# Optimization experiments

Measured on AMD Instinct MI355X. Metric: run time of the kernel, lower is better.

The kernel has to match this reference:

```python
import jax, jax.numpy as jnp
import numpy as np
from jax import lax

K = 3  # deform kernel size (forced by shape consistency of the offset branch)


def conv2d(x, w, b, pad):
    y = lax.conv_general_dilated(x, w, (1, 1), [(pad, pad), (pad, pad)],
                                 dimension_numbers=('NCHW', 'OIHW', 'NCHW'))
    return y + b[None, :, None, None]


def deform_conv(x, offset, w):
    # Deformable conv v1, stride 1, pad 0, per-group offsets, zero outside borders.
    B, Cin, H, W = x.shape
    Cout = w.shape[0]
    Ho, Wo = H - K + 1, W - K + 1
    G = offset.shape[1] // (2 * K * K)  # num deformable groups (= cin // c_p_g)
    cpg = Cin // G
    # offset layout: [B, G, K*K, 2(y,x), Ho, Wo]
    off = offset.reshape(B, G, K * K, 2, Ho, Wo)
    ky = (jnp.arange(K * K) // K).astype(x.dtype)
    kx = (jnp.arange(K * K) % K).astype(x.dtype)
    py = off[:, :, :, 0] + jnp.arange(Ho, dtype=x.dtype)[None, None, None, :, None] + ky[None, None, :, None, None]
    px = off[:, :, :, 1] + jnp.arange(Wo, dtype=x.dtype)[None, None, None, None, :] + kx[None, None, :, None, None]
    y0 = jnp.floor(py)
    x0 = jnp.floor(px)
    fy = (py - y0)[..., None]  # [B,G,KK,Ho,Wo,1]
    fx = (px - x0)[..., None]
    y0i = y0.astype(jnp.int32)
    x0i = x0.astype(jnp.int32)
    xr = x.reshape(B, G, cpg, H, W)
    bi = jnp.arange(B)[:, None, None, None, None]
    gi = jnp.arange(G)[None, :, None, None, None]

    def gather(iy, ix):
        valid = (iy >= 0) & (iy < H) & (ix >= 0) & (ix < W)
        v = xr[bi, gi, :, jnp.clip(iy, 0, H - 1), jnp.clip(ix, 0, W - 1)]  # [B,G,KK,Ho,Wo,cpg]
        return v * valid[..., None].astype(x.dtype)

    v = ((1 - fy) * (1 - fx) * gather(y0i, x0i)
         + (1 - fy) * fx * gather(y0i, x0i + 1)
         + fy * (1 - fx) * gather(y0i + 1, x0i)
         + fy * fx * gather(y0i + 1, x0i + 1))
    # [B,G,KK,Ho,Wo,cpg] -> [B, Cin*K*K, Ho, Wo] matching weight layout [Cout, Cin, K, K]
    cols = v.transpose(0, 1, 5, 2, 3, 4).reshape(B, Cin * K * K, Ho, Wo)
    return jnp.einsum('ok,bkhw->bohw', w.reshape(Cout, -1), cols)


def setup_inputs() -> dict:
    key = jax.random.key(0)
    ks = jax.random.split(key, 8)
    B, cin, cout, H, W = 4, 64, 64, 130, 130
    s = 0.05
    x = jax.random.normal(ks[0], (B, cin, H, W), jnp.float32)
    w0 = jax.random.normal(ks[1], (cin, cin, 3, 3), jnp.float32) * s
    b0 = jnp.zeros((cin,), jnp.float32)
    w1 = jax.random.normal(ks[2], (cin // 2, cin, 1, 1), jnp.float32) * s
    b1 = jnp.zeros((cin // 2,), jnp.float32)
    w2 = jax.random.normal(ks[3], (cin // 2, cin // 2, 3, 3), jnp.float32) * s
    b2 = jnp.zeros((cin // 2,), jnp.float32)
    off_ch = cin * 2 * K * K  # c_p_g = 1 -> G = cin
    w3 = jax.random.normal(ks[4], (off_ch, cin // 2, 1, 1), jnp.float32) * s
    b3 = jnp.zeros((off_ch,), jnp.float32)
    wd = jax.random.normal(ks[5], (cout, cin, K, K), jnp.float32) * s
    return {"x": x, "w0": w0, "b0": b0, "w1": w1, "b1": b1, "w2": w2, "b2": b2,
            "w3": w3, "b3": b3, "wd": wd}


def reference(x, w0, b0, w1, b1, w2, b2, w3, b3, wd):
    t = conv2d(x, w0, b0, 0)                                   # [B,cin,H-2,W-2]
    t = lax.reduce_window(t, -jnp.inf, lax.max, (1, 1, 2, 2), (1, 1, 2, 2), 'VALID')
    t = conv2d(t, w1, b1, 0)
    t = conv2d(t, w2, b2, 1)
    t = conv2d(t, w3, b3, 0)                                   # offset logits
    t = jnp.repeat(jnp.repeat(t, 2, axis=2), 2, axis=3)        # nearest x2 upsample
    return deform_conv(x, t, wd)
```

## Files before the change

### kernel.cpp

```cpp
#include <hip/hip_runtime.h>
#include <hip/hip_bf16.h>
#include <hip/hip_fp16.h>


#define HX 130
#define WX 130

typedef short bf16x8 __attribute__((ext_vector_type(8)));
typedef _Float16 f16x8 __attribute__((ext_vector_type(8)));
typedef float f32x4 __attribute__((ext_vector_type(4)));

static __device__ __forceinline__ unsigned short f2bf(float f) {
    unsigned u = __float_as_uint(f);
    unsigned r = u + 0x7fff + ((u >> 16) & 1);
    return (unsigned short)(r >> 16);
}

static __device__ __forceinline__ int aoff(int row, int col) {
    return row * 320 + ((((col >> 3) ^ (row & 7))) << 3) + (col & 7);
}

__global__ __launch_bounds__(256) void k_wdt(const float* __restrict__ wd,
                                             const float* __restrict__ w3,
                                             unsigned short* __restrict__ wdtb,
                                             __half* __restrict__ w3h) {
    int idx = blockIdx.x * 256 + threadIdx.x;
    if (idx < 36864) {
        int o = idx / 576;
        int rem = idx - o * 576;
        int c = rem / 9;
        int kk = rem - c * 9;
        int h = c >> 5;
        int c5 = c & 31;
        int col = (c5 >> 4) * 144 + ((c5 >> 3) & 1) * 72 + (c5 & 7) * 9 + kk;
        wdtb[(size_t)(h * 64 + o) * 288 + col] = f2bf(wd[idx]);
    } else {
        int i2 = idx - 36864;
        if (i2 < 36864) w3h[i2] = __float2half_rn(w3[i2]);
    }
}

__global__ __launch_bounds__(256, 4) void k_conv0_pool(const float* __restrict__ x,
                                                       const float* __restrict__ w0,
                                                       const float* __restrict__ b0,
                                                       float* __restrict__ p1) {
    int idx = blockIdx.x;
    int tile = idx & 15;
    int cog = (idx >> 4) & 15;
    int b = idx >> 8;
    int tid = threadIdx.x;
    int pw = tid & 63;
    int phl = tid >> 6;
    int ph = tile * 4 + phl;
    __shared__ float slab[2][10 * WX];
    const float* xb = x + (size_t)(b * 64) * HX * WX;
    int row0 = tile * 8;
    const float* xbase = xb + row0 * WX;
    float acc[4][4];
    #pragma unroll
    for (int i = 0; i < 4; ++i)
        #pragma unroll
        for (int j = 0; j < 4; ++j) acc[i][j] = 0.f;

    float pre[11];
    #pragma unroll
    for (int j = 0; j < 11; ++j) {
        int i = tid + j * 256;
        int ci = i / 1300, off = i - ci * 1300;
        pre[j] = (i < 2600) ? xbase[(size_t)ci * (HX * WX) + off] : 0.f;
    }

    for (int cg = 0; cg < 32; ++cg) {
        __syncthreads();
        #pragma unroll
        for (int j = 0; j < 11; ++j) {
            int i = tid + j * 256;
            if (i < 2600) ((float*)slab)[i] = pre[j];
        }
        __syncthreads();
        if (cg < 31) {
            const float* xp = xbase + (size_t)(2 * cg + 2) * (HX * WX);
            #pragma unroll
            for (int j = 0; j < 11; ++j) {
                int i = tid + j * 256;
                int ci = i / 1300, off = i - ci * 1300;
                pre[j] = (i < 2600) ? xp[(size_t)ci * (HX * WX) + off] : 0.f;
            }
        }
        #pragma unroll
        for (int lc = 0; lc < 2; ++lc) {
            int ci = 2 * cg + lc;
            float v[4][4];
            #pragma unroll
            for (int r2 = 0; r2 < 4; ++r2) {
                const float* rp = &slab[lc][(2 * phl + r2) * WX + 2 * pw];
                float2 a = *(const float2*)rp;
                float2 bb = *(const float2*)(rp + 2);
                v[r2][0] = a.x; v[r2][1] = a.y; v[r2][2] = bb.x; v[r2][3] = bb.y;
            }
            #pragma unroll
            for (int i = 0; i < 4; ++i) {
                const float* wp = w0 + (((cog * 4 + i) * 64) + ci) * 9;
                float w[9];
                #pragma unroll
                for (int k = 0; k < 9; ++k) w[k] = wp[k];
                #pragma unroll
                for (int dr = 0; dr < 2; ++dr)
                    #pragma unroll
                    for (int dc = 0; dc < 2; ++dc) {
                        float s = acc[i][dr * 2 + dc];
                        #pragma unroll
                        for (int ky = 0; ky < 3; ++ky)
                            #pragma unroll
                            for (int kx = 0; kx < 3; ++kx)
                                s += w[ky * 3 + kx] * v[dr + ky][dc + kx];
                        acc[i][dr * 2 + dc] = s;
                    }
            }
        }
    }
    #pragma unroll
    for (int i = 0; i < 4; ++i) {
        float m = fmaxf(fmaxf(acc[i][0], acc[i][1]), fmaxf(acc[i][2], acc[i][3]))
                + b0[cog * 4 + i];
        p1[(((size_t)b * 64 + cog * 4 + i) * 64 + ph) * 64 + pw] = m;
    }
}

__global__ __launch_bounds__(256) void k_conv1x1_a(const float* __restrict__ p1,
                                                   const float* __restrict__ w1,
                                                   const float* __restrict__ b1,
                                                   float* __restrict__ t2) {
    int blk = blockIdx.x;
    int pt = blk & 15;
    int cog = (blk >> 4) & 15;
    int b = blk >> 8;
    int p = pt * 256 + threadIdx.x;
    float acc[2];
    #pragma unroll
    for (int i = 0; i < 2; ++i) acc[i] = b1[cog * 2 + i];
    const float* ip = p1 + (size_t)b * 64 * 4096 + p;
    for (int ci = 0; ci < 64; ++ci) {
        float v = ip[(size_t)ci * 4096];
        #pragma unroll
        for (int i = 0; i < 2; ++i) acc[i] += w1[(cog * 2 + i) * 64 + ci] * v;
    }
    float* op = t2 + (size_t)b * 32 * 4096 + p;
    #pragma unroll
    for (int i = 0; i < 2; ++i) op[(size_t)(cog * 2 + i) * 4096] = acc[i];
}

__global__ __launch_bounds__(256) void k_conv3x3_b(const float* __restrict__ t2,
                                                   const float* __restrict__ w2,
                                                   const float* __restrict__ b2,
                                                   float* __restrict__ t3) {
    int blk = blockIdx.x;
    int pt = blk & 15;
    int cog = (blk >> 4) & 15;
    int b = blk >> 8;
    int p = pt * 256 + threadIdx.x;
    int hy = p >> 6, wx = p & 63;
    float acc[2];
    #pragma unroll
    for (int i = 0; i < 2; ++i) acc[i] = b2[cog * 2 + i];
    const float* ip = t2 + (size_t)b * 32 * 4096;
    for (int ci = 0; ci < 32; ++ci) {
        float v[9];
        #pragma unroll
        for (int ky = 0; ky < 3; ++ky) {
            int yy = hy + ky - 1;
            #pragma unroll
            for (int kx = 0; kx < 3; ++kx) {
                int xx = wx + kx - 1;
                bool ok = (yy >= 0 && yy < 64 && xx >= 0 && xx < 64);
                int yc = min(max(yy, 0), 63), xc = min(max(xx, 0), 63);
                float val = ip[(size_t)ci * 4096 + yc * 64 + xc];
                v[ky * 3 + kx] = ok ? val : 0.f;
            }
        }
        #pragma unroll
        for (int i = 0; i < 2; ++i) {
            const float* wp = w2 + (((cog * 2 + i) * 32) + ci) * 9;
            float s = acc[i];
            #pragma unroll
            for (int k = 0; k < 9; ++k) s += wp[k] * v[k];
            acc[i] = s;
        }
    }
    float* op = t3 + (size_t)b * 32 * 4096 + p;
    #pragma unroll
    for (int i = 0; i < 2; ++i) op[(size_t)(cog * 2 + i) * 4096] = acc[i];
}

__global__ __launch_bounds__(256, 3) void k_deform(const float* __restrict__ x,
                                                   const float* __restrict__ t3,
                                                   const __half* __restrict__ w3h,
                                                   const float* __restrict__ b3,
                                                   const unsigned short* __restrict__ wdtb,
                                                   float* __restrict__ out) {
    int blk = blockIdx.x;
    int b = blk & 3;
    int strip = blk >> 2;
    int tid = threadIdx.x;
    int po0 = strip * 16;
    int qy = po0 >> 6;
    int qx0 = po0 & 63;
    int w = tid >> 6;
    int lane = tid & 63;
    int lm = lane & 15;
    int lq = lane >> 4;
    int tq = tid & 15;
    int kb = tid >> 4;

    __shared__ __align__(16) unsigned short alds[64 * 320];
    __shared__ __align__(16) __half2 soff[2304];
    __shared__ __align__(16) _Float16 st3t[16 * 40];

    f32x4 acc[4];
    #pragma unroll
    for (int n = 0; n < 4; ++n) acc[n] = (f32x4){0.f, 0.f, 0.f, 0.f};

    const float* xb = x + (size_t)b * 64 * HX * WX;
    float fybase = (float)(2 * qy);
    float fxbase = (float)(2 * (qx0 + tq));

    {
        int px = tid & 15, ci0 = tid >> 4;
        const float* t3p = t3 + (size_t)b * 32 * 4096 + (qy * 64 + qx0 + px);
        st3t[px * 40 + ci0]      = (_Float16)t3p[(size_t)ci0 * 4096];
        st3t[px * 40 + ci0 + 16] = (_Float16)t3p[(size_t)(ci0 + 16) * 4096];
    }
    __syncthreads();
    const f16x8 bfrag = *(const f16x8*)&st3t[lm * 40 + lq * 8];

    for (int h = 0; h < 2; ++h) {
        #pragma unroll 1
        for (int sl = 0; sl < 2; ++sl) {
            int s = h * 2 + sl;
            __syncthreads();

            #pragma unroll
            for (int rep = 0; rep < 5; ++rep) {
                int t = rep * 4 + w;
                if (rep == 4) { if (w >= 2) break; t = 16 + w; }
                const f16x8 afrag = *(const f16x8*)((const _Float16*)w3h
                        + (size_t)(s * 288 + t * 16 + lm) * 32 + lq * 8);
                f32x4 d = __builtin_amdgcn_mfma_f32_16x16x32_f16(
                        afrag, bfrag, (f32x4){0.f, 0.f, 0.f, 0.f}, 0, 0, 0);
                float4 bq = *(const float4*)(b3 + s * 288 + t * 16 + lq * 4);
                int p0 = (t * 8 + lq * 2) * 16 + lm;
                soff[p0]      = __floats2half2_rn(d[0] + bq.x, d[1] + bq.y);
                soff[p0 + 16] = __floats2half2_rn(d[2] + bq.z, d[3] + bq.w);
            }
            __syncthreads();

            __half2 o2h[9];
            #pragma unroll
            for (int it = 0; it < 9; ++it)
                o2h[it] = soff[it * 256 + tid];
            #pragma unroll
            for (int it = 0; it < 9; ++it) {
                int kcol = it * 16 + kb;
                int lc = kcol >= 72;
                int ckk = kcol - 72 * lc;
                int ch = (ckk * 57) >> 9;
                int kk = ckk - ch * 9;
                int c = s * 16 + lc * 8 + ch;
                int clocal = sl * 144 + kcol;
                float2 off = __half22float2(o2h[it]);
                float py = off.x + fybase + (float)(kk / 3);
                float px = off.y + fxbase + (float)(kk % 3);
                float y0f = floorf(py), x0f = floorf(px);
                float fy = py - y0f, fx = px - x0f;
                int y0 = (int)y0f, x0 = (int)x0f;
                const float* xp = xb + (size_t)c * (HX * WX);
                float tv[3][3];
                bool fastok = (y0 >= 0) & (y0 <= HX - 3) & (x0 >= 0) & (x0 <= WX - 3);
                if (__all(fastok)) {
                    int xe = x0 & ~1;
                    int odd = x0 & 1;
                    const float* rp = xp + y0 * WX + xe;
                    #pragma unroll
                    for (int r = 0; r < 3; ++r) {
                        float2 A = *(const float2*)(rp);
                        float2 B = *(const float2*)(rp + 2);
                        tv[r][0] = odd ? A.y : A.x;
                        tv[r][1] = odd ? B.x : A.y;
                        tv[r][2] = odd ? B.y : B.x;
                        rp += WX;
                    }
                } else {
                    #pragma unroll
                    for (int r = 0; r < 3; ++r) {
                        int yy = y0 + r;
                        bool vy = (yy >= 0) & (yy < HX);
                        int yc = min(max(yy, 0), HX - 1);
                        #pragma unroll
                        for (int sx = 0; sx < 3; ++sx) {
                            int xx = x0 + sx;
                            bool vx = (xx >= 0) & (xx < WX);
                            int xc = min(max(xx, 0), WX - 1);
                            float val = xp[yc * WX + xc];
                            tv[r][sx] = (vy & vx) ? val : 0.f;
                        }
                    }
                }
                float h0[3], h1[3];
                #pragma unroll
                for (int r = 0; r < 3; ++r) {
                    h0[r] = tv[r][0] + fx * (tv[r][1] - tv[r][0]);
                    h1[r] = tv[r][1] + fx * (tv[r][2] - tv[r][1]);
                }
                alds[aoff(0 * 16 + tq, clocal)] = f2bf(h0[0] + fy * (h0[1] - h0[0]));
                alds[aoff(1 * 16 + tq, clocal)] = f2bf(h1[0] + fy * (h1[1] - h1[0]));
                alds[aoff(2 * 16 + tq, clocal)] = f2bf(h0[1] + fy * (h0[2] - h0[1]));
                alds[aoff(3 * 16 + tq, clocal)] = f2bf(h1[1] + fy * (h1[2] - h1[1]));
            }
        }
        __syncthreads();

        int arow = w * 16 + lm;
        const unsigned short* bbase = wdtb + (size_t)(h * 64) * 288;
        #pragma unroll
        for (int ks = 0; ks < 9; ++ks) {
            bf16x8 a = *(const bf16x8*)&alds[aoff(arow, ks * 32 + lq * 8)];
            #pragma unroll
            for (int n = 0; n < 4; ++n) {
                bf16x8 bb = *(const bf16x8*)(bbase + (size_t)(n * 16 + lm) * 288
                                             + ks * 32 + lq * 8);
                acc[n] = __builtin_amdgcn_mfma_f32_16x16x32_bf16(a, bb, acc[n], 0, 0, 0);
            }
        }
    }

    __syncthreads();
    float* dlds = (float*)alds;
    #pragma unroll
    for (int n = 0; n < 4; ++n) {
        int oc = n * 16 + lm;
        #pragma unroll
        for (int r = 0; r < 4; ++r) {
            int px = w * 16 + lq * 4 + r;
            dlds[oc * 65 + px] = acc[n][r];
        }
    }
    __syncthreads();
    {
        int oc = tid >> 2;
        int sy = (tid >> 1) & 1;
        int qh = (tid & 1) * 8;
        float* orow = out + (((size_t)b * 64 + oc) * 128 + 2 * qy + sy) * 128 + 2 * qx0;
        const float* d0 = &dlds[oc * 65 + (sy * 2 + 0) * 16];
        const float* d1 = &dlds[oc * 65 + (sy * 2 + 1) * 16];
        #pragma unroll
        for (int i = 0; i < 8; ++i) {
            int q = qh + i;
            *(float2*)(orow + 2 * q) = make_float2(d0[q], d1[q]);
        }
    }
}

extern "C" void kernel_launch(void* const* d_in, const int* in_sizes, int n_in,
                              void* d_out, int out_size, void* d_ws, size_t ws_size,
                              hipStream_t stream) {
    const float* x  = (const float*)d_in[0];
    const float* w0 = (const float*)d_in[1];
    const float* b0 = (const float*)d_in[2];
    const float* w1 = (const float*)d_in[3];
    const float* b1 = (const float*)d_in[4];
    const float* w2 = (const float*)d_in[5];
    const float* b2 = (const float*)d_in[6];
    const float* w3 = (const float*)d_in[7];
    const float* b3 = (const float*)d_in[8];
    const float* wd = (const float*)d_in[9];
    float* out = (float*)d_out;

    float* ws = (float*)d_ws;
    float* p1    = ws;
    float* t2    = p1 + 1048576;
    float* t3    = t2 + 524288;
    unsigned short* wdtb = (unsigned short*)(t3 + 524288);
    __half* w3h = (__half*)(wdtb + 36864);

    k_wdt<<<288, 256, 0, stream>>>(wd, w3, wdtb, w3h);
    k_conv0_pool<<<1024, 256, 0, stream>>>(x, w0, b0, p1);
    k_conv1x1_a<<<1024, 256, 0, stream>>>(p1, w1, b1, t2);
    k_conv3x3_b<<<1024, 256, 0, stream>>>(t2, w2, b2, t3);
    k_deform<<<1024, 256, 0, stream>>>(x, t3, w3h, b3, wdtb, out);
}
```

Before: 250.0 us.

## Rewrite conv0+maxpool as bf16 MFMA implicit GEMM with im2col in LDS

Replaces the scalar FP32 3x3 conv0+2x2 maxpool kernel with an implicit-GEMM version. Each block builds an im2col tile of 64 pixels by 144 columns (16 input channels by 9 taps) in swizzled LDS as bf16 and multiplies it against pre-packed bf16 weights using 16x16x32 MFMA. The pool and bias are applied from an LDS staging tile. This trades FP32 accuracy for bf16 and adds weight packing to the prep kernel, aiming to remove the FP32 FMA bottleneck of conv0.

```diff
diff --git a/kernel.cpp b/kernel.cpp
--- a/kernel.cpp
+++ b/kernel.cpp
@@ -16,14 +16,20 @@
     return (unsigned short)(r >> 16);
 }
 
-static __device__ __forceinline__ int aoff(int row, int col) {
+static __device__ __forceinline__ int aoff320(int row, int col) {
     return row * 320 + ((((col >> 3) ^ (row & 7))) << 3) + (col & 7);
+}
+
+static __device__ __forceinline__ int aoff192(int row, int col) {
+    return row * 192 + ((((col >> 3) ^ (row & 7))) << 3) + (col & 7);
 }
 
 __global__ __launch_bounds__(256) void k_wdt(const float* __restrict__ wd,
                                              const float* __restrict__ w3,
+                                             const float* __restrict__ w0,
                                              unsigned short* __restrict__ wdtb,
-                                             __half* __restrict__ w3h) {
+                                             __half* __restrict__ w3h,
+                                             unsigned short* __restrict__ w0b) {
     int idx = blockIdx.x * 256 + threadIdx.x;
     if (idx < 36864) {
         int o = idx / 576;
@@ -34,96 +40,117 @@
         int c5 = c & 31;
         int col = (c5 >> 4) * 144 + ((c5 >> 3) & 1) * 72 + (c5 & 7) * 9 + kk;
         wdtb[(size_t)(h * 64 + o) * 288 + col] = f2bf(wd[idx]);
+        if (idx < 16) wdtb[36864 + idx] = 0;
+    } else if (idx < 73728) {
+        int i2 = idx - 36864;
+        w3h[i2] = __float2half_rn(w3[i2]);
     } else {
-        int i2 = idx - 36864;
-        if (i2 < 36864) w3h[i2] = __float2half_rn(w3[i2]);
-    }
-}
-
-__global__ __launch_bounds__(256, 4) void k_conv0_pool(const float* __restrict__ x,
-                                                       const float* __restrict__ w0,
+        int i3 = idx - 73728;
+        int row = i3 / 160;
+        int col = i3 - row * 160;
+        int cig = row >> 6, oc = row & 63;
+        unsigned short v = 0;
+        if (col < 144) {
+            int ci = (col * 57) >> 9;
+            int kk = col - ci * 9;
+            v = f2bf(w0[(size_t)(oc * 64 + cig * 16 + ci) * 9 + kk]);
+        }
+        w0b[i3] = v;
+    }
+}
+
+__global__ __launch_bounds__(256, 4) void k_conv0_mfma(const float* __restrict__ x,
+                                                       const unsigned short* __restrict__ w0b,
                                                        const float* __restrict__ b0,
                                                        float* __restrict__ p1) {
-    int idx = blockIdx.x;
-    int tile = idx & 15;
-    int cog = (idx >> 4) & 15;
-    int b = idx >> 8;
+    int blk = blockIdx.x;
+    int tx = blk & 15;
+    int ty = (blk >> 4) & 15;
+    int b = blk >> 8;
     int tid = threadIdx.x;
-    int pw = tid & 63;
-    int phl = tid >> 6;
-    int ph = tile * 4 + phl;
-    __shared__ float slab[2][10 * WX];
-    const float* xb = x + (size_t)(b * 64) * HX * WX;
-    int row0 = tile * 8;
-    const float* xbase = xb + row0 * WX;
-    float acc[4][4];
-    #pragma unroll
-    for (int i = 0; i < 4; ++i)
-        #pragma unroll
-        for (int j = 0; j < 4; ++j) acc[i][j] = 0.f;
-
-    float pre[11];
-    #pragma unroll
-    for (int j = 0; j < 11; ++j) {
-        int i = tid + j * 256;
-        int ci = i / 1300, off = i - ci * 1300;
-        pre[j] = (i < 2600) ? xbase[(size_t)ci * (HX * WX) + off] : 0.f;
-    }
-
-    for (int cg = 0; cg < 32; ++cg) {
+    int w = tid >> 6;
+    int lane = tid & 63;
+    int lm = lane & 15;
+    int lq = lane >> 4;
+    int oy0 = ty * 8, ox0 = tx * 8;
+
+    __shared__ __align__(16) unsigned short alds[64 * 192];
+    __shared__ __align__(16) float xlds[1600];
+
+    f32x4 acc[4];
+    #pragma unroll
+    for (int n = 0; n < 4; ++n) acc[n] = (f32x4){0.f, 0.f, 0.f, 0.f};
+
+    if (tid < 128) {
+        *(bf16x8*)&alds[aoff192(tid >> 1, 144 + (tid & 1) * 8)] =
+            (bf16x8){0, 0, 0, 0, 0, 0, 0, 0};
+    }
+
+    const float* xb = x + (size_t)(b * 64) * (HX * WX) + oy0 * WX + ox0;
+    int apx = tid >> 2;
+    int acq = tid & 3;
+    int py = apx >> 3, pxx = apx & 7;
+
+    for (int cig = 0; cig < 4; ++cig) {
+        #pragma unroll
+        for (int j = 0; j < 7; ++j) {
+            int i = tid + j * 256;
+            if (i < 1600) {
+                int ci = i / 100;
+                int rem = i - ci * 100;
+                int rr = rem / 10, cc = rem - rr * 10;
+                xlds[i] = xb[(size_t)(cig * 16 + ci) * (HX * WX) + rr * WX + cc];
+            }
+        }
         __syncthreads();
         #pragma unroll
-        for (int j = 0; j < 11; ++j) {
-            int i = tid + j * 256;
-            if (i < 2600) ((float*)slab)[i] = pre[j];
+        for (int jj = 0; jj < 36; ++jj) {
+            int col = acq * 36 + jj;
+            int ci = (col * 57) >> 9;
+            int kk = col - ci * 9;
+            int ky = kk / 3, kx = kk - ky * 3;
+            alds[aoff192(apx, col)] =
+                f2bf(xlds[ci * 100 + (py + ky) * 10 + (pxx + kx)]);
         }
         __syncthreads();
-        if (cg < 31) {
-            const float* xp = xbase + (size_t)(2 * cg + 2) * (HX * WX);
-            #pragma unroll
-            for (int j = 0; j < 11; ++j) {
-                int i = tid + j * 256;
-                int ci = i / 1300, off = i - ci * 1300;
-                pre[j] = (i < 2600) ? xp[(size_t)ci * (HX * WX) + off] : 0.f;
-            }
-        }
-        #pragma unroll
-        for (int lc = 0; lc < 2; ++lc) {
-            int ci = 2 * cg + lc;
-            float v[4][4];
-            #pragma unroll
-            for (int r2 = 0; r2 < 4; ++r2) {
-                const float* rp = &slab[lc][(2 * phl + r2) * WX + 2 * pw];
-                float2 a = *(const float2*)rp;
-                float2 bb = *(const float2*)(rp + 2);
-                v[r2][0] = a.x; v[r2][1] = a.y; v[r2][2] = bb.x; v[r2][3] = bb.y;
-            }
-            #pragma unroll
-            for (int i = 0; i < 4; ++i) {
-                const float* wp = w0 + (((cog * 4 + i) * 64) + ci) * 9;
-                float w[9];
-                #pragma unroll
-                for (int k = 0; k < 9; ++k) w[k] = wp[k];
-                #pragma unroll
-                for (int dr = 0; dr < 2; ++dr)
-                    #pragma unroll
-                    for (int dc = 0; dc < 2; ++dc) {
-                        float s = acc[i][dr * 2 + dc];
-                        #pragma unroll
-                        for (int ky = 0; ky < 3; ++ky)
-                            #pragma unroll
-                            for (int kx = 0; kx < 3; ++kx)
-                                s += w[ky * 3 + kx] * v[dr + ky][dc + kx];
-                        acc[i][dr * 2 + dc] = s;
-                    }
-            }
-        }
-    }
-    #pragma unroll
-    for (int i = 0; i < 4; ++i) {
-        float m = fmaxf(fmaxf(acc[i][0], acc[i][1]), fmaxf(acc[i][2], acc[i][3]))
-                + b0[cog * 4 + i];
-        p1[(((size_t)b * 64 + cog * 4 + i) * 64 + ph) * 64 + pw] = m;
+        int arow = w * 16 + lm;
+        const unsigned short* bbase = w0b + (size_t)cig * 64 * 160;
+        #pragma unroll
+        for (int ks = 0; ks < 5; ++ks) {
+            bf16x8 a = *(const bf16x8*)&alds[aoff192(arow, ks * 32 + lq * 8)];
+            #pragma unroll
+            for (int n = 0; n < 4; ++n) {
+                bf16x8 bb = *(const bf16x8*)(bbase + (size_t)(n * 16 + lm) * 160
+                                             + ks * 32 + lq * 8);
+                acc[n] = __builtin_amdgcn_mfma_f32_16x16x32_bf16(a, bb, acc[n], 0, 0, 0);
+            }
+        }
+    }
+
+    __syncthreads();
+    float* dlds = (float*)alds;
+    #pragma unroll
+    for (int n = 0; n < 4; ++n) {
+        int oc = n * 16 + lm;
+        #pragma unroll
+        for (int r = 0; r < 4; ++r) {
+            int px = w * 16 + lq * 4 + r;
+            dlds[oc * 65 + px] = acc[n][r];
+        }
+    }
+    __syncthreads();
+    {
+        int oc = tid >> 2;
+        int ppy = tid & 3;
+        float bo = b0[oc];
+        float4 o4;
+        #pragma unroll
+        for (int ppx = 0; ppx < 4; ++ppx) {
+            const float* dp = &dlds[oc * 65 + (2 * ppy) * 8 + 2 * ppx];
+            float m = fmaxf(fmaxf(dp[0], dp[1]), fmaxf(dp[8], dp[9])) + bo;
+            ((float*)&o4)[ppx] = m;
+        }
+        *(float4*)(p1 + (((size_t)b * 64 + oc) * 64 + ty * 4 + ppy) * 64 + tx * 4) = o4;
     }
 }
 
@@ -311,10 +338,10 @@
                     h0[r] = tv[r][0] + fx * (tv[r][1] - tv[r][0]);
                     h1[r] = tv[r][1] + fx * (tv[r][2] - tv[r][1]);
                 }
-                alds[aoff(0 * 16 + tq, clocal)] = f2bf(h0[0] + fy * (h0[1] - h0[0]));
-                alds[aoff(1 * 16 + tq, clocal)] = f2bf(h1[0] + fy * (h1[1] - h1[0]));
-                alds[aoff(2 * 16 + tq, clocal)] = f2bf(h0[1] + fy * (h0[2] - h0[1]));
-                alds[aoff(3 * 16 + tq, clocal)] = f2bf(h1[1] + fy * (h1[2] - h1[1]));
+                alds[aoff320(0 * 16 + tq, clocal)] = f2bf(h0[0] + fy * (h0[1] - h0[0]));
+                alds[aoff320(1 * 16 + tq, clocal)] = f2bf(h1[0] + fy * (h1[1] - h1[0]));
+                alds[aoff320(2 * 16 + tq, clocal)] = f2bf(h0[1] + fy * (h0[2] - h0[1]));
+                alds[aoff320(3 * 16 + tq, clocal)] = f2bf(h1[1] + fy * (h1[2] - h1[1]));
             }
         }
         __syncthreads();
@@ -323,7 +350,7 @@
         const unsigned short* bbase = wdtb + (size_t)(h * 64) * 288;
         #pragma unroll
         for (int ks = 0; ks < 9; ++ks) {
-            bf16x8 a = *(const bf16x8*)&alds[aoff(arow, ks * 32 + lq * 8)];
+            bf16x8 a = *(const bf16x8*)&alds[aoff320(arow, ks * 32 + lq * 8)];
             #pragma unroll
             for (int n = 0; n < 4; ++n) {
                 bf16x8 bb = *(const bf16x8*)(bbase + (size_t)(n * 16 + lm) * 288
@@ -380,10 +407,11 @@
     float* t2    = p1 + 1048576;
     float* t3    = t2 + 524288;
     unsigned short* wdtb = (unsigned short*)(t3 + 524288);
-    __half* w3h = (__half*)(wdtb + 36864);
-
-    k_wdt<<<288, 256, 0, stream>>>(wd, w3, wdtb, w3h);
-    k_conv0_pool<<<1024, 256, 0, stream>>>(x, w0, b0, p1);
+    __half* w3h = (__half*)(wdtb + 36880);
+    unsigned short* w0b = (unsigned short*)(w3h + 36864);
+
+    k_wdt<<<448, 256, 0, stream>>>(wd, w3, w0, wdtb, w3h, w0b);
+    k_conv0_mfma<<<1024, 256, 0, stream>>>(x, w0b, b0, p1);
     k_conv1x1_a<<<1024, 256, 0, stream>>>(p1, w1, b1, t2);
     k_conv3x3_b<<<1024, 256, 0, stream>>>(t2, w2, b2, t3);
     k_deform<<<1024, 256, 0, stream>>>(x, t3, w3h, b3, wdtb, out);
```

New measurement: 226.8 us. 9.3% less time.
